# Kernel optimization log

Measured on AMD Instinct MI355X. Metric: run time of the kernel, lower is better.

Reference implementation:

```python
import jax, jax.numpy as jnp
import numpy as np

B, T, L = 256, 1024, 128  # batch, seq_len, num_labels


def setup_inputs() -> dict:
    key = jax.random.key(0)
    k1, k2, k3, k4, k5 = jax.random.split(key, 5)
    h = jax.random.normal(k1, (B, T, L), dtype=jnp.float32)
    labels = jax.random.randint(k2, (B, T), 0, L)
    mask = jnp.ones((B, T), dtype=jnp.float32)
    u = lambda k, s: jax.random.uniform(k, s, jnp.float32, -0.1, 0.1)
    trans_matrix = u(k3, (L, L))
    start_trans = u(k4, (L,))
    end_trans = u(k5, (L,))
    return {"h": h, "labels": labels, "mask": mask,
            "trans_matrix": trans_matrix, "start_trans": start_trans,
            "end_trans": end_trans}


def reference(h, labels, mask, trans_matrix, start_trans, end_trans):
    # ---- numerator: score of the gold path ----
    h_y = jnp.take_along_axis(h, labels[..., None], axis=2)[..., 0]      # (B,T)
    trans_y = trans_matrix[labels[:, :-1], labels[:, 1:]]                # (B,T-1)
    num = start_trans[labels[:, 0]]
    num = num + jnp.sum(h_y[:, :-1] * mask[:, :-1] + trans_y * mask[:, 1:], axis=1)
    last_idx = mask.astype(jnp.int32).sum(axis=1) - 1                    # (B,)
    last_labels = jnp.take_along_axis(labels, last_idx[:, None], axis=1)[:, 0]
    # original torch code gathers from h[:, -1] (last timestep), keep faithful
    num = num + jnp.take_along_axis(h[:, -1], last_labels[:, None], axis=1)[:, 0] * mask[:, -1]
    num = num + end_trans[last_labels]

    # ---- denominator: log partition via scan over time ----
    def step(score, inp):
        h_t, m_t = inp  # (B,L), (B,)
        s = jax.nn.logsumexp(score[:, :, None] + h_t[:, None, :] + trans_matrix[None], axis=1)
        m = m_t[:, None]
        return s * m + score * (1.0 - m), None

    score0 = start_trans[None, :] + h[:, 0]                              # (B,L)
    hs = jnp.swapaxes(h, 0, 1)[1:]                                       # (T-1,B,L)
    ms = mask.T[1:]                                                      # (T-1,B)
    scoreT, _ = jax.lax.scan(step, score0, (hs, ms))
    den = jax.nn.logsumexp(scoreT + end_trans[None, :], axis=1)          # (B,)

    return num - den
```

## Files before the change

### kernel.cpp

```cpp
#include <hip/hip_runtime.h>
#include <math.h>

#define Bb 256
#define Tt 1024
#define Ll 128

typedef float v2f __attribute__((ext_vector_type(2)));

__device__ __forceinline__ v2f ev2(float a, float b) { v2f r; r.x = a; r.y = b; return r; }

__global__ __launch_bounds__(256)
__attribute__((amdgpu_waves_per_eu(1, 1)))
void crf_fused_kernel(
    const float* __restrict__ h, const int* __restrict__ labels,
    const float* __restrict__ mask, const float* __restrict__ trans,
    const float* __restrict__ start_trans, const float* __restrict__ end_trans,
    float* __restrict__ out)
{
    __shared__ float p_lds[2][160];
    __shared__ float mk_lds[Tt + 4];
    __shared__ float redm[4], reds[4], racc[4], rmsum[4];

    const int b = blockIdx.x;
    const int tid = threadIdx.x;
    const int wave = tid >> 6;
    const int lane = tid & 63;
    const int jgrp = lane >> 3;
    const int isl  = lane & 7;
    const int jbase = (wave << 5) + (jgrp << 2);
    const int wcol  = jbase + (isl & 3);
    const bool writer = (isl < 4);
    const int waddr = wcol + ((wcol >> 4) << 2);
    const bool lb0 = (lane & 1) != 0;
    const bool lb1 = (lane & 2) != 0;

    const float* hb = h + (size_t)b * Tt * Ll;
    const float* mk = mask + b * Tt;
    const int* lab = labels + b * Tt;

    ((float4*)mk_lds)[tid] = ((const float4*)mk)[tid];

    float nacc = 0.f, nms = 0.f;
    #pragma unroll
    for (int r = 0; r < 4; ++r) {
        int t = tid + (r << 8);
        float mt = mk[t];
        nms += mt;
        if (t < Tt - 1) {
            int lt = lab[t], lt1 = lab[t + 1];
            nacc += hb[t * Ll + lt] * mt + trans[lt * Ll + lt1] * mk[t + 1];
        }
    }

    const float* tp = trans + (size_t)(isl << 4) * Ll + jbase;
#define EXT2(k, c) ev2(__expf(tp[(2 * (k)) * Ll + (c)]), __expf(tp[(2 * (k) + 1) * Ll + (c)]))
    v2f EA0=EXT2(0,0),EA1=EXT2(1,0),EA2=EXT2(2,0),EA3=EXT2(3,0),
        EA4=EXT2(4,0),EA5=EXT2(5,0),EA6=EXT2(6,0),EA7=EXT2(7,0);
    v2f EB0=EXT2(0,1),EB1=EXT2(1,1),EB2=EXT2(2,1),EB3=EXT2(3,1),
        EB4=EXT2(4,1),EB5=EXT2(5,1),EB6=EXT2(6,1),EB7=EXT2(7,1);
    v2f EC0=EXT2(0,2),EC1=EXT2(1,2),EC2=EXT2(2,2),EC3=EXT2(3,2),
        EC4=EXT2(4,2),EC5=EXT2(5,2),EC6=EXT2(6,2),EC7=EXT2(7,2);
    v2f ED0=EXT2(0,3),ED1=EXT2(1,3),ED2=EXT2(2,3),ED3=EXT2(3,3),
        ED4=EXT2(4,3),ED5=EXT2(5,3),ED6=EXT2(6,3),ED7=EXT2(7,3);
#undef EXT2

    float S = start_trans[0] + hb[0] + 16.0f;
    float score0 = start_trans[wcol] + hb[wcol];
    float pw = __expf(score0 - S);
    if (writer) p_lds[0][waddr] = pw;

    float h1 = hb[1 * Ll + wcol], m1 = mk[1];
    float h2 = hb[2 * Ll + wcol], m2 = mk[2];
    float h3 = hb[3 * Ll + wcol], m3 = mk[3];
    float h0 = hb[4 * Ll + wcol], m0 = mk[4];
    __syncthreads();

    float ex1 = __expf(h1) * m1, om1 = 1.f - m1;
    float ex0, om0, ex2, om2, ex3, om3;
    float4 MQ;

#define DPPA(x, ctrl) __int_as_float(__builtin_amdgcn_update_dpp( \
        0, __float_as_int(x), ctrl, 0xF, 0xF, true))

#define BODY(RBUF, UPD, EXc, OMc, HN, MN, EXn, OMn, HR, MR, TR, MV, LQ) {  \
    const float4* pp = (const float4*)(&p_lds[RBUF][isl * 20]);        \
    float4 Q0 = pp[0], Q1 = pp[1], Q2 = pp[2], Q3 = pp[3];             \
    float pz = 0.f;                                                    \
    if (UPD) pz = p_lds[RBUF][0];                                      \
    HR = hb[(TR) * Ll + wcol];                                         \
    MR = (MV);                                                         \
    if (LQ) MQ = *(const float4*)(&mk_lds[(TR) + 1]);                  \
    v2f q00 = {Q0.x,Q0.y}, q01 = {Q0.z,Q0.w};                          \
    v2f q10 = {Q1.x,Q1.y}, q11 = {Q1.z,Q1.w};                          \
    v2f q20 = {Q2.x,Q2.y}, q21 = {Q2.z,Q2.w};                          \
    v2f q30 = {Q3.x,Q3.y}, q31 = {Q3.z,Q3.w};                          \
    v2f A0 = q00*EA0; A0 = q01*EA1 + A0; A0 = q10*EA2 + A0;            \
    A0 = q11*EA3 + A0; A0 = q20*EA4 + A0; A0 = q21*EA5 + A0;           \
    A0 = q30*EA6 + A0; A0 = q31*EA7 + A0;                              \
    v2f A1 = q00*EB0; A1 = q01*EB1 + A1; A1 = q10*EB2 + A1;            \
    A1 = q11*EB3 + A1; A1 = q20*EB4 + A1; A1 = q21*EB5 + A1;           \
    A1 = q30*EB6 + A1; A1 = q31*EB7 + A1;                              \
    v2f A2 = q00*EC0; A2 = q01*EC1 + A2; A2 = q10*EC2 + A2;            \
    A2 = q11*EC3 + A2; A2 = q20*EC4 + A2; A2 = q21*EC5 + A2;           \
    A2 = q30*EC6 + A2; A2 = q31*EC7 + A2;                              \
    v2f A3 = q00*ED0; A3 = q01*ED1 + A3; A3 = q10*ED2 + A3;            \
    A3 = q11*ED3 + A3; A3 = q20*ED4 + A3; A3 = q21*ED5 + A3;           \
    A3 = q30*ED6 + A3; A3 = q31*ED7 + A3;                              \
    float a0 = A0.x + A0.y, a1 = A1.x + A1.y;                          \
    float a2 = A2.x + A2.y, a3 = A3.x + A3.y;                          \
    a0 += DPPA(a0, 0x141); a1 += DPPA(a1, 0x141);                      \
    a2 += DPPA(a2, 0x141); a3 += DPPA(a3, 0x141);                      \
    float u01 = lb0 ? a1 : a0, v01 = lb0 ? a0 : a1;                    \
    float b01 = u01 + DPPA(v01, 0xB1);                                 \
    float u23 = lb0 ? a3 : a2, v23 = lb0 ? a2 : a3;                    \
    float b23 = u23 + DPPA(v23, 0xB1);                                 \
    float uf = lb1 ? b23 : b01, vf = lb1 ? b01 : b23;                  \
    float acc = uf + DPPA(vf, 0x4E);                                   \
    float c1 = EXc, c0 = pw * OMc;                                     \
    if (UPD) { float ed = __fdividef(1.12535175e-7f, pz);              \
               c1 *= ed; c0 *= ed; S += __logf(pz) + 16.0f; }          \
    float pn = fmaf(acc, c1, c0);                                      \
    if (writer) p_lds[(RBUF) ^ 1][waddr] = pn;                         \
    EXn = __expf(HN) * MN; OMn = 1.f - MN;                             \
    pw = pn;                                                           \
    __builtin_amdgcn_sched_barrier(0);                                 \
    asm volatile("s_waitcnt lgkmcnt(0)");                              \
    __builtin_amdgcn_s_barrier();                                      \
    __builtin_amdgcn_sched_barrier(0);                                 \
}

    BODY(0, 0, ex1, om1, h2, m2, ex2, om2, h1, m1, 5, mk_lds[5], 0)
    BODY(1, 0, ex2, om2, h3, m3, ex3, om3, h2, m2, 6, mk_lds[6], 0)
    BODY(0, 0, ex3, om3, h0, m0, ex0, om0, h3, m3, 7, mk_lds[7], 1)

    for (int k = 1; k < 255; ++k) {
        int t4 = k << 2;
        BODY(1, 1, ex0, om0, h1, m1, ex1, om1, h0, m0, t4 + 4, MQ.x, 0)
        BODY(0, 0, ex1, om1, h2, m2, ex2, om2, h1, m1, t4 + 5, MQ.y, 0)
        BODY(1, 0, ex2, om2, h3, m3, ex3, om3, h2, m2, t4 + 6, MQ.z, 0)
        BODY(0, 0, ex3, om3, h0, m0, ex0, om0, h3, m3, t4 + 7, MQ.w, 1)
    }
    BODY(1, 1, ex0, om0, h1, m1, ex1, om1, h0, m0, Tt - 4, MQ.x, 0)
    BODY(0, 0, ex1, om1, h2, m2, ex2, om2, h1, m1, Tt - 1, MQ.y, 0)
    BODY(1, 0, ex2, om2, h3, m3, ex3, om3, h2, m2, Tt - 1, MQ.z, 0)
    BODY(0, 0, ex3, om3, h0, m0, ex0, om0, h3, m3, Tt - 1, MQ.w, 0)
#undef BODY
#undef DPPA

    float v = __logf(pw) + S + end_trans[wcol];
    float mval = writer ? v : -1e30f;
    #pragma unroll
    for (int off = 32; off; off >>= 1) {
        mval = fmaxf(mval, __shfl_xor(mval, off, 64));
        nacc += __shfl_down(nacc, off, 64);
        nms  += __shfl_down(nms,  off, 64);
    }
    if (lane == 0) { redm[wave] = mval; racc[wave] = nacc; rmsum[wave] = nms; }
    __syncthreads();
    float M = fmaxf(fmaxf(redm[0], redm[1]), fmaxf(redm[2], redm[3]));
    float e = writer ? __expf(v - M) : 0.f;
    #pragma unroll
    for (int off = 32; off; off >>= 1) e += __shfl_xor(e, off, 64);
    if (lane == 0) reds[wave] = e;
    __syncthreads();
    if (tid == 0) {
        float den = M + __logf(reds[0] + reds[1] + reds[2] + reds[3]);
        float a  = racc[0] + racc[1] + racc[2] + racc[3];
        float mm = rmsum[0] + rmsum[1] + rmsum[2] + rmsum[3];
        int last_idx = (int)(mm + 0.5f) - 1;
        if (last_idx < 0) last_idx = 0;
        if (last_idx > Tt - 1) last_idx = Tt - 1;
        int last_lab = lab[last_idx];
        float num = a + start_trans[lab[0]];
        num += hb[(Tt - 1) * Ll + last_lab] * mk_lds[Tt - 1];
        num += end_trans[last_lab];
        out[b] = num - den;
    }
}

extern "C" void kernel_launch(void* const* d_in, const int* in_sizes, int n_in,
                              void* d_out, int out_size, void* d_ws, size_t ws_size,
                              hipStream_t stream) {
    const float* h           = (const float*)d_in[0];
    const int*   labels      = (const int*)d_in[1];
    const float* mask        = (const float*)d_in[2];
    const float* trans       = (const float*)d_in[3];
    const float* start_trans = (const float*)d_in[4];
    const float* end_trans   = (const float*)d_in[5];
    float* out = (float*)d_out;

    crf_fused_kernel<<<Bb, 256, 0, stream>>>(h, labels, mask, trans,
                                             start_trans, end_trans, out);
}
```

Measured before the change: 247.8 us.

## Compute CRF forward recurrence matvec with bf16 MFMA instead of packed FP32 FMAs

Replaces the per-step 128x128 exp(trans) matrix-vector product, previously done with packed FP32 FMAs and DPP reductions, with eight bf16 MFMA 16x16x32 instructions per wave. The exp(trans) tiles are converted to bf16 and held in registers, and the probability vector is stored in LDS as bf16. The A operand is the broadcast vector, so only row 0 of each MFMA output is used. This removes the DPP cross-lane reduction and most of the FMA work on the serial critical path. In exchange it adds MFMA latency on each step and bf16 rounding of the recurrence state, which risks accuracy drift over 1024 steps.

```diff
diff --git a/kernel.cpp b/kernel.cpp
--- a/kernel.cpp
+++ b/kernel.cpp
@@ -1,13 +1,22 @@
 #include <hip/hip_runtime.h>
+#include <hip/hip_bf16.h>
 #include <math.h>
 
 #define Bb 256
 #define Tt 1024
 #define Ll 128
 
-typedef float v2f __attribute__((ext_vector_type(2)));
+typedef short s8v  __attribute__((ext_vector_type(8)));
+typedef float f32x4 __attribute__((ext_vector_type(4)));
 
-__device__ __forceinline__ v2f ev2(float a, float b) { v2f r; r.x = a; r.y = b; return r; }
+__device__ __forceinline__ short f2bf(float x) {
+    unsigned u = __float_as_uint(x);
+    unsigned r = (u + 0x7FFFu + ((u >> 16) & 1u)) >> 16;
+    return (short)r;
+}
+__device__ __forceinline__ float bf2f(unsigned short u) {
+    return __uint_as_float(((unsigned)u) << 16);
+}
 
 __global__ __launch_bounds__(256)
 __attribute__((amdgpu_waves_per_eu(1, 1)))
@@ -17,7 +26,7 @@
     const float* __restrict__ start_trans, const float* __restrict__ end_trans,
     float* __restrict__ out)
 {
-    __shared__ float p_lds[2][160];
+    __shared__ __align__(16) unsigned short pbuf[2][Ll];
     __shared__ float mk_lds[Tt + 4];
     __shared__ float redm[4], reds[4], racc[4], rmsum[4];
 
@@ -25,14 +34,12 @@
     const int tid = threadIdx.x;
     const int wave = tid >> 6;
     const int lane = tid & 63;
-    const int jgrp = lane >> 3;
-    const int isl  = lane & 7;
-    const int jbase = (wave << 5) + (jgrp << 2);
-    const int wcol  = jbase + (isl & 3);
-    const bool writer = (isl < 4);
-    const int waddr = wcol + ((wcol >> 4) << 2);
-    const bool lb0 = (lane & 1) != 0;
-    const bool lb1 = (lane & 2) != 0;
+    const int l15 = lane & 15;
+    const int l4  = lane >> 4;
+    const int w32 = wave << 5;
+    const bool wr16 = (lane < 16);
+    const int jT0 = w32 + l15;
+    const int jT1 = w32 + 16 + l15;
 
     const float* hb = h + (size_t)b * Tt * Ll;
     const float* mk = mask + b * Tt;
@@ -52,103 +59,93 @@
         }
     }
 
-    const float* tp = trans + (size_t)(isl << 4) * Ll + jbase;
-#define EXT2(k, c) ev2(__expf(tp[(2 * (k)) * Ll + (c)]), __expf(tp[(2 * (k) + 1) * Ll + (c)]))
-    v2f EA0=EXT2(0,0),EA1=EXT2(1,0),EA2=EXT2(2,0),EA3=EXT2(3,0),
-        EA4=EXT2(4,0),EA5=EXT2(5,0),EA6=EXT2(6,0),EA7=EXT2(7,0);
-    v2f EB0=EXT2(0,1),EB1=EXT2(1,1),EB2=EXT2(2,1),EB3=EXT2(3,1),
-        EB4=EXT2(4,1),EB5=EXT2(5,1),EB6=EXT2(6,1),EB7=EXT2(7,1);
-    v2f EC0=EXT2(0,2),EC1=EXT2(1,2),EC2=EXT2(2,2),EC3=EXT2(3,2),
-        EC4=EXT2(4,2),EC5=EXT2(5,2),EC6=EXT2(6,2),EC7=EXT2(7,2);
-    v2f ED0=EXT2(0,3),ED1=EXT2(1,3),ED2=EXT2(2,3),ED3=EXT2(3,3),
-        ED4=EXT2(4,3),ED5=EXT2(5,3),ED6=EXT2(6,3),ED7=EXT2(7,3);
-#undef EXT2
+#define MKB(c, J) ({ const float* tb = trans + (size_t)((c) * 32 + l4 * 8) * Ll + (J); \
+    s8v r_; r_[0]=f2bf(__expf(tb[0]));      r_[1]=f2bf(__expf(tb[Ll]));     \
+            r_[2]=f2bf(__expf(tb[2*Ll]));   r_[3]=f2bf(__expf(tb[3*Ll]));   \
+            r_[4]=f2bf(__expf(tb[4*Ll]));   r_[5]=f2bf(__expf(tb[5*Ll]));   \
+            r_[6]=f2bf(__expf(tb[6*Ll]));   r_[7]=f2bf(__expf(tb[7*Ll])); r_; })
+    s8v B00 = MKB(0, jT0), B01 = MKB(1, jT0), B02 = MKB(2, jT0), B03 = MKB(3, jT0);
+    s8v B10 = MKB(0, jT1), B11 = MKB(1, jT1), B12 = MKB(2, jT1), B13 = MKB(3, jT1);
+#undef MKB
 
     float S = start_trans[0] + hb[0] + 16.0f;
-    float score0 = start_trans[wcol] + hb[wcol];
-    float pw = __expf(score0 - S);
-    if (writer) p_lds[0][waddr] = pw;
+    if (tid < Ll) {
+        float sc0 = start_trans[tid] + hb[tid];
+        pbuf[0][tid] = (unsigned short)f2bf(__expf(sc0 - S));
+    }
+    float pwA = __expf(start_trans[jT0] + hb[jT0] - S);
+    float pwB = __expf(start_trans[jT1] + hb[jT1] - S);
 
-    float h1 = hb[1 * Ll + wcol], m1 = mk[1];
-    float h2 = hb[2 * Ll + wcol], m2 = mk[2];
-    float h3 = hb[3 * Ll + wcol], m3 = mk[3];
-    float h0 = hb[4 * Ll + wcol], m0 = mk[4];
+    float h1a = hb[1 * Ll + jT0], h1b = hb[1 * Ll + jT1], m1 = mk[1];
+    float h2a = hb[2 * Ll + jT0], h2b = hb[2 * Ll + jT1], m2 = mk[2];
+    float h3a = hb[3 * Ll + jT0], h3b = hb[3 * Ll + jT1], m3 = mk[3];
+    float h0a = hb[4 * Ll + jT0], h0b = hb[4 * Ll + jT1], m0 = mk[4];
     __syncthreads();
 
-    float ex1 = __expf(h1) * m1, om1 = 1.f - m1;
-    float ex0, om0, ex2, om2, ex3, om3;
+    float ex1a = __expf(h1a) * m1, ex1b = __expf(h1b) * m1, om1 = 1.f - m1;
+    float ex0a, ex0b, om0, ex2a, ex2b, om2, ex3a, ex3b, om3;
     float4 MQ;
+    const f32x4 Zac = {0.f, 0.f, 0.f, 0.f};
 
-#define DPPA(x, ctrl) __int_as_float(__builtin_amdgcn_update_dpp( \
-        0, __float_as_int(x), ctrl, 0xF, 0xF, true))
-
-#define BODY(RBUF, UPD, EXc, OMc, HN, MN, EXn, OMn, HR, MR, TR, MV, LQ) {  \
-    const float4* pp = (const float4*)(&p_lds[RBUF][isl * 20]);        \
-    float4 Q0 = pp[0], Q1 = pp[1], Q2 = pp[2], Q3 = pp[3];             \
-    float pz = 0.f;                                                    \
-    if (UPD) pz = p_lds[RBUF][0];                                      \
-    HR = hb[(TR) * Ll + wcol];                                         \
-    MR = (MV);                                                         \
-    if (LQ) MQ = *(const float4*)(&mk_lds[(TR) + 1]);                  \
-    v2f q00 = {Q0.x,Q0.y}, q01 = {Q0.z,Q0.w};                          \
-    v2f q10 = {Q1.x,Q1.y}, q11 = {Q1.z,Q1.w};                          \
-    v2f q20 = {Q2.x,Q2.y}, q21 = {Q2.z,Q2.w};                          \
-    v2f q30 = {Q3.x,Q3.y}, q31 = {Q3.z,Q3.w};                          \
-    v2f A0 = q00*EA0; A0 = q01*EA1 + A0; A0 = q10*EA2 + A0;            \
-    A0 = q11*EA3 + A0; A0 = q20*EA4 + A0; A0 = q21*EA5 + A0;           \
-    A0 = q30*EA6 + A0; A0 = q31*EA7 + A0;                              \
-    v2f A1 = q00*EB0; A1 = q01*EB1 + A1; A1 = q10*EB2 + A1;            \
-    A1 = q11*EB3 + A1; A1 = q20*EB4 + A1; A1 = q21*EB5 + A1;           \
-    A1 = q30*EB6 + A1; A1 = q31*EB7 + A1;                              \
-    v2f A2 = q00*EC0; A2 = q01*EC1 + A2; A2 = q10*EC2 + A2;            \
-    A2 = q11*EC3 + A2; A2 = q20*EC4 + A2; A2 = q21*EC5 + A2;           \
-    A2 = q30*EC6 + A2; A2 = q31*EC7 + A2;                              \
-    v2f A3 = q00*ED0; A3 = q01*ED1 + A3; A3 = q10*ED2 + A3;            \
-    A3 = q11*ED3 + A3; A3 = q20*ED4 + A3; A3 = q21*ED5 + A3;           \
-    A3 = q30*ED6 + A3; A3 = q31*ED7 + A3;                              \
-    float a0 = A0.x + A0.y, a1 = A1.x + A1.y;                          \
-    float a2 = A2.x + A2.y, a3 = A3.x + A3.y;                          \
-    a0 += DPPA(a0, 0x141); a1 += DPPA(a1, 0x141);                      \
-    a2 += DPPA(a2, 0x141); a3 += DPPA(a3, 0x141);                      \
-    float u01 = lb0 ? a1 : a0, v01 = lb0 ? a0 : a1;                    \
-    float b01 = u01 + DPPA(v01, 0xB1);                                 \
-    float u23 = lb0 ? a3 : a2, v23 = lb0 ? a2 : a3;                    \
-    float b23 = u23 + DPPA(v23, 0xB1);                                 \
-    float uf = lb1 ? b23 : b01, vf = lb1 ? b01 : b23;                  \
-    float acc = uf + DPPA(vf, 0x4E);                                   \
-    float c1 = EXc, c0 = pw * OMc;                                     \
-    if (UPD) { float ed = __fdividef(1.12535175e-7f, pz);              \
-               c1 *= ed; c0 *= ed; S += __logf(pz) + 16.0f; }          \
-    float pn = fmaf(acc, c1, c0);                                      \
-    if (writer) p_lds[(RBUF) ^ 1][waddr] = pn;                         \
-    EXn = __expf(HN) * MN; OMn = 1.f - MN;                             \
-    pw = pn;                                                           \
-    __builtin_amdgcn_sched_barrier(0);                                 \
-    asm volatile("s_waitcnt lgkmcnt(0)");                              \
-    __builtin_amdgcn_s_barrier();                                      \
-    __builtin_amdgcn_sched_barrier(0);                                 \
+#define BODY(RBUF, UPD, EXcA, EXcB, OMc, HNa, HNb, MN, EXnA, EXnB, OMn,  \
+             HRa, HRb, MR, TR, MV, LQ) {                                 \
+    const unsigned short* pb_ = pbuf[RBUF];                              \
+    s8v a0 = *(const s8v*)(pb_ + l4 * 8);                                \
+    s8v a1 = *(const s8v*)(pb_ + 32 + l4 * 8);                           \
+    s8v a2 = *(const s8v*)(pb_ + 64 + l4 * 8);                           \
+    s8v a3 = *(const s8v*)(pb_ + 96 + l4 * 8);                           \
+    float pz = 0.f;                                                      \
+    if (UPD) pz = bf2f(pb_[0]);                                          \
+    HRa = hb[(TR) * Ll + jT0];                                           \
+    HRb = hb[(TR) * Ll + jT1];                                           \
+    MR = (MV);                                                           \
+    if (LQ) MQ = *(const float4*)(&mk_lds[(TR) + 1]);                    \
+    f32x4 ac0 = __builtin_amdgcn_mfma_f32_16x16x32_bf16(a0, B00, Zac, 0, 0, 0); \
+    ac0 = __builtin_amdgcn_mfma_f32_16x16x32_bf16(a1, B01, ac0, 0, 0, 0);\
+    ac0 = __builtin_amdgcn_mfma_f32_16x16x32_bf16(a2, B02, ac0, 0, 0, 0);\
+    ac0 = __builtin_amdgcn_mfma_f32_16x16x32_bf16(a3, B03, ac0, 0, 0, 0);\
+    f32x4 ac1 = __builtin_amdgcn_mfma_f32_16x16x32_bf16(a0, B10, Zac, 0, 0, 0); \
+    ac1 = __builtin_amdgcn_mfma_f32_16x16x32_bf16(a1, B11, ac1, 0, 0, 0);\
+    ac1 = __builtin_amdgcn_mfma_f32_16x16x32_bf16(a2, B12, ac1, 0, 0, 0);\
+    ac1 = __builtin_amdgcn_mfma_f32_16x16x32_bf16(a3, B13, ac1, 0, 0, 0);\
+    float s0 = ac0[0], s1 = ac1[0];                                      \
+    float c1a = EXcA, c1b = EXcB;                                        \
+    float c0a = pwA * OMc, c0b = pwB * OMc;                              \
+    if (UPD) { float ed = __fdividef(1.12535175e-7f, pz);                \
+               c1a *= ed; c1b *= ed; c0a *= ed; c0b *= ed;               \
+               S += __logf(pz) + 16.0f; }                                \
+    float pnA = fmaf(s0, c1a, c0a);                                      \
+    float pnB = fmaf(s1, c1b, c0b);                                      \
+    if (wr16) { pbuf[(RBUF) ^ 1][w32 + l15]      = (unsigned short)f2bf(pnA); \
+                pbuf[(RBUF) ^ 1][w32 + 16 + l15] = (unsigned short)f2bf(pnB); } \
+    EXnA = __expf(HNa) * MN; EXnB = __expf(HNb) * MN; OMn = 1.f - MN;    \
+    pwA = pnA; pwB = pnB;                                                \
+    __builtin_amdgcn_sched_barrier(0);                                   \
+    asm volatile("s_waitcnt lgkmcnt(0)");                                \
+    __builtin_amdgcn_s_barrier();                                        \
+    __builtin_amdgcn_sched_barrier(0);                                   \
 }
 
-    BODY(0, 0, ex1, om1, h2, m2, ex2, om2, h1, m1, 5, mk_lds[5], 0)
-    BODY(1, 0, ex2, om2, h3, m3, ex3, om3, h2, m2, 6, mk_lds[6], 0)
-    BODY(0, 0, ex3, om3, h0, m0, ex0, om0, h3, m3, 7, mk_lds[7], 1)
+    BODY(0, 0, ex1a, ex1b, om1, h2a, h2b, m2, ex2a, ex2b, om2, h1a, h1b, m1, 5, mk_lds[5], 0)
+    BODY(1, 0, ex2a, ex2b, om2, h3a, h3b, m3, ex3a, ex3b, om3, h2a, h2b, m2, 6, mk_lds[6], 0)
+    BODY(0, 0, ex3a, ex3b, om3, h0a, h0b, m0, ex0a, ex0b, om0, h3a, h3b, m3, 7, mk_lds[7], 1)
 
     for (int k = 1; k < 255; ++k) {
         int t4 = k << 2;
-        BODY(1, 1, ex0, om0, h1, m1, ex1, om1, h0, m0, t4 + 4, MQ.x, 0)
-        BODY(0, 0, ex1, om1, h2, m2, ex2, om2, h1, m1, t4 + 5, MQ.y, 0)
-        BODY(1, 0, ex2, om2, h3, m3, ex3, om3, h2, m2, t4 + 6, MQ.z, 0)
-        BODY(0, 0, ex3, om3, h0, m0, ex0, om0, h3, m3, t4 + 7, MQ.w, 1)
+        BODY(1, 1, ex0a, ex0b, om0, h1a, h1b, m1, ex1a, ex1b, om1, h0a, h0b, m0, t4 + 4, MQ.x, 0)
+        BODY(0, 0, ex1a, ex1b, om1, h2a, h2b, m2, ex2a, ex2b, om2, h1a, h1b, m1, t4 + 5, MQ.y, 0)
+        BODY(1, 0, ex2a, ex2b, om2, h3a, h3b, m3, ex3a, ex3b, om3, h2a, h2b, m2, t4 + 6, MQ.z, 0)
+        BODY(0, 0, ex3a, ex3b, om3, h0a, h0b, m0, ex0a, ex0b, om0, h3a, h3b, m3, t4 + 7, MQ.w, 1)
     }
-    BODY(1, 1, ex0, om0, h1, m1, ex1, om1, h0, m0, Tt - 4, MQ.x, 0)
-    BODY(0, 0, ex1, om1, h2, m2, ex2, om2, h1, m1, Tt - 1, MQ.y, 0)
-    BODY(1, 0, ex2, om2, h3, m3, ex3, om3, h2, m2, Tt - 1, MQ.z, 0)
-    BODY(0, 0, ex3, om3, h0, m0, ex0, om0, h3, m3, Tt - 1, MQ.w, 0)
+    BODY(1, 1, ex0a, ex0b, om0, h1a, h1b, m1, ex1a, ex1b, om1, h0a, h0b, m0, Tt - 1, MQ.x, 0)
+    BODY(0, 0, ex1a, ex1b, om1, h2a, h2b, m2, ex2a, ex2b, om2, h1a, h1b, m1, Tt - 1, MQ.y, 0)
+    BODY(1, 0, ex2a, ex2b, om2, h3a, h3b, m3, ex3a, ex3b, om3, h2a, h2b, m2, Tt - 1, MQ.z, 0)
+    BODY(0, 0, ex3a, ex3b, om3, h0a, h0b, m0, ex0a, ex0b, om0, h3a, h3b, m3, Tt - 1, MQ.w, 0)
 #undef BODY
-#undef DPPA
 
-    float v = __logf(pw) + S + end_trans[wcol];
-    float mval = writer ? v : -1e30f;
+    float v0 = __logf(pwA) + S + end_trans[jT0];
+    float v1 = __logf(pwB) + S + end_trans[jT1];
+    float mval = wr16 ? fmaxf(v0, v1) : -1e30f;
     #pragma unroll
     for (int off = 32; off; off >>= 1) {
         mval = fmaxf(mval, __shfl_xor(mval, off, 64));
@@ -158,7 +155,7 @@
     if (lane == 0) { redm[wave] = mval; racc[wave] = nacc; rmsum[wave] = nms; }
     __syncthreads();
     float M = fmaxf(fmaxf(redm[0], redm[1]), fmaxf(redm[2], redm[3]));
-    float e = writer ? __expf(v - M) : 0.f;
+    float e = wr16 ? (__expf(v0 - M) + __expf(v1 - M)) : 0.f;
     #pragma unroll
     for (int off = 32; off; off >>= 1) e += __shfl_xor(e, off, 64);
     if (lane == 0) reds[wave] = e;
```

New measurement: 238.5 us. -3.7%, faster.
